# Performance work log

Hardware: AMD Instinct MI355X
Metric: run time of the kernel (lower is better)

## Reference

```python
import jax, jax.numpy as jnp
import numpy as np

N = 50000
E = 800000
F0, F1, F2 = 256, 128, 64
EPS = 1e-5


def setup_inputs() -> dict:
    key = jax.random.key(0)
    ks = jax.random.split(key, 20)
    x = jax.random.normal(ks[0], (N, F0), dtype=jnp.float32)
    src = jax.random.randint(ks[1], (E,), 0, N)
    dst = jax.random.randint(ks[2], (E,), 0, N)
    edge_index = jnp.stack([src, dst]).astype(jnp.int64)

    def lin(k, fi, fo):
        s = 1.0 / np.sqrt(fi)
        k1, k2 = jax.random.split(k)
        W = jax.random.uniform(k1, (fi, fo), minval=-s, maxval=s, dtype=jnp.float32)
        b = jax.random.uniform(k2, (fo,), minval=-s, maxval=s, dtype=jnp.float32)
        return W, b

    We1, be1 = lin(ks[3], F0, F1)
    We2, be2 = lin(ks[4], F1, F2)
    Wd1, bd1 = lin(ks[5], F2, F1)
    Wd2, bd2 = lin(ks[6], F1, F0)
    return {
        'x': x, 'edge_index': edge_index,
        'We1': We1, 'be1': be1, 'g1': jnp.ones((F1,)), 'bb1': jnp.zeros((F1,)),
        'We2': We2, 'be2': be2, 'g2': jnp.ones((F2,)), 'bb2': jnp.zeros((F2,)),
        'Wd1': Wd1, 'bd1': bd1, 'g3': jnp.ones((F1,)), 'bb3': jnp.zeros((F1,)),
        'Wd2': Wd2, 'bd2': bd2, 'g4': jnp.ones((F0,)), 'bb4': jnp.zeros((F0,)),
    }


def _gcn(x, W, b, src, dst, dinv_src_dst, dinv_self):
    # PyG GCNConv: linear first, then sym-normalized propagation with self-loops
    h = x @ W + b                               # [N, Fout]
    msg = h[src] * dinv_src_dst[:, None]        # [E, Fout]
    out = jax.ops.segment_sum(msg, dst, num_segments=N)
    return out + h * dinv_self[:, None]         # self-loop term


def _bn(x, g, b):
    # BatchNorm1d training-mode: biased batch stats over node dim
    m = jnp.mean(x, axis=0)
    v = jnp.mean(jnp.square(x - m), axis=0)
    return g * (x - m) * jax.lax.rsqrt(v + EPS) + b


def reference(x, edge_index, We1, be1, g1, bb1, We2, be2, g2, bb2,
              Wd1, bd1, g3, bb3, Wd2, bd2, g4, bb4):
    src, dst = edge_index[0], edge_index[1]
    deg = jnp.zeros((N,), x.dtype).at[dst].add(1.0) + 1.0  # in-degree + self-loop
    dinv = jax.lax.rsqrt(deg)
    dsd = dinv[src] * dinv[dst]
    dself = dinv * dinv

    relu = jax.nn.relu
    # Encoder block 0 (outer i==0): relu(GCN), relu(BN)
    h = relu(_gcn(x, We1, be1, src, dst, dsd, dself))
    h = relu(_bn(h, g1, bb1))
    enc1 = h
    # Encoder block 1 (outer i==1 == len(inner)-1): relu(GCN), BN (no relu)
    h = relu(_gcn(h, We2, be2, src, dst, dsd, dself))
    h = _bn(h, g2, bb2)
    enc2 = h
    # Decoder block 0: relu(GCN), relu(BN)
    h = relu(_gcn(h, Wd1, bd1, src, dst, dsd, dself))
    h = relu(_bn(h, g3, bb3))
    # Decoder block 1 (i==1): relu(GCN), BN (no relu)
    h = relu(_gcn(h, Wd2, bd2, src, dst, dsd, dself))
    h = _bn(h, g4, bb4)
    # AE returns (reconstruction, encoded_embeddings)
    return h, enc1, enc2
```

## Files before the change

kernel.cpp:

```cpp
#include <hip/hip_runtime.h>
#include <hip/hip_fp16.h>

#define N_NODES 50000
#define F0 256
#define F1 128
#define F2 64
#define BN_EPS 1e-5f

typedef float f32x4 __attribute__((ext_vector_type(4)));
typedef __bf16 bf16x8 __attribute__((ext_vector_type(8)));
typedef unsigned short ushort8v __attribute__((ext_vector_type(8)));

__device__ __forceinline__ float bflo(unsigned v) { return __uint_as_float(v << 16); }
__device__ __forceinline__ float bfhi(unsigned v) { return __uint_as_float(v & 0xFFFF0000u); }
__device__ __forceinline__ unsigned short f2bf(float f) {
  unsigned u = __float_as_uint(f);
  u += 0x7FFFu + ((u >> 16) & 1u);
  return (unsigned short)(u >> 16);
}
__device__ __forceinline__ void split2(float a, unsigned short& hi, unsigned short& lo) {
  hi = f2bf(a);
  float hf = __uint_as_float((unsigned)hi << 16);
  lo = f2bf(a - hf);
}
__device__ __forceinline__ int rdl(int v, int l) { return __builtin_amdgcn_readlane(v, l); }
__device__ __forceinline__ float h2f(unsigned short h) {
  __half hh = *reinterpret_cast<__half*>(&h);
  return __half2float(hh);
}
__device__ __forceinline__ unsigned short f2h(float f) {
  __half hh = __float2half(f);
  return *reinterpret_cast<unsigned short*>(&hh);
}

__global__ void count_dst(const int* __restrict__ dst, int* __restrict__ counts,
                          int* __restrict__ eslot, int E) {
  int e = blockIdx.x * blockDim.x + threadIdx.x;
  if (e < E) eslot[e] = atomicAdd(&counts[dst[e]], 1);
}

__global__ __launch_bounds__(256) void scan_blocks(const int* __restrict__ counts,
                                                   int* __restrict__ offs,
                                                   int* __restrict__ bsum,
                                                   float* __restrict__ dinv) {
  __shared__ int s_w[4];
  const int tid = threadIdx.x, lane = tid & 63, wid = tid >> 6;
  const int base = blockIdx.x * 1024 + tid * 4;
  int v0 = 0, v1 = 0, v2 = 0, v3 = 0;
  if (base + 3 < N_NODES) {
    int4 v = *(const int4*)(counts + base);
    v0 = v.x; v1 = v.y; v2 = v.z; v3 = v.w;
  } else if (base < N_NODES) {
    v0 = counts[base];
    if (base + 1 < N_NODES) v1 = counts[base + 1];
    if (base + 2 < N_NODES) v2 = counts[base + 2];
  }
  if (base < N_NODES) {
    dinv[base] = rsqrtf((float)v0 + 1.0f);
    if (base + 1 < N_NODES) dinv[base + 1] = rsqrtf((float)v1 + 1.0f);
    if (base + 2 < N_NODES) dinv[base + 2] = rsqrtf((float)v2 + 1.0f);
    if (base + 3 < N_NODES) dinv[base + 3] = rsqrtf((float)v3 + 1.0f);
  }
  int t = v0 + v1 + v2 + v3;
  int incl = t;
#pragma unroll
  for (int d = 1; d < 64; d <<= 1) {
    int x = __shfl_up(incl, d);
    if (lane >= d) incl += x;
  }
  if (lane == 63) s_w[wid] = incl;
  __syncthreads();
  int woff = 0;
#pragma unroll
  for (int j = 0; j < 4; j++)
    if (j < wid) woff += s_w[j];
  int p = woff + incl - t;
  if (base < N_NODES) offs[base] = p;
  p += v0;
  if (base + 1 < N_NODES) offs[base + 1] = p;
  p += v1;
  if (base + 2 < N_NODES) offs[base + 2] = p;
  p += v2;
  if (base + 3 < N_NODES) offs[base + 3] = p;
  if (tid == 255) bsum[blockIdx.x] = woff + incl;
}

__global__ void scan_tops(int* __restrict__ bsum, int* __restrict__ offs, int nblk) {
  int lane = threadIdx.x;
  int v = (lane < nblk) ? bsum[lane] : 0;
  int incl = v;
#pragma unroll
  for (int d = 1; d < 64; d <<= 1) {
    int x = __shfl_up(incl, d);
    if (lane >= d) incl += x;
  }
  if (lane < nblk) bsum[lane] = incl - v;
  if (lane == 63) offs[N_NODES] = incl;
}

__global__ __launch_bounds__(256) void scan_add(int* __restrict__ offs,
                                                const int* __restrict__ bsum) {
  const int add = bsum[blockIdx.x];
  const int base = blockIdx.x * 1024 + threadIdx.x * 4;
  if (base + 3 < N_NODES) {
    int4 v = *(const int4*)(offs + base);
    v.x += add; v.y += add; v.z += add; v.w += add;
    *(int4*)(offs + base) = v;
  } else if (base < N_NODES) {
    offs[base] += add;
    if (base + 1 < N_NODES) offs[base + 1] += add;
    if (base + 2 < N_NODES) offs[base + 2] += add;
  }
}

__global__ void fill_csr(const int* __restrict__ src, const int* __restrict__ dst,
                         const int* __restrict__ offs, const int* __restrict__ eslot,
                         const float* __restrict__ dinv,
                         unsigned* __restrict__ csrU, int E) {
  int e = blockIdx.x * blockDim.x + threadIdx.x;
  if (e < E) {
    int s = src[e], d = dst[e];
    int p = offs[d] + eslot[e];
    unsigned ent = (unsigned)s | ((unsigned)f2h(dinv[s]) << 16);
    __builtin_nontemporal_store(ent, &csrU[p]);
  }
}

__global__ void compute_rowsum(const int* __restrict__ offs,
                               const unsigned* __restrict__ csrU,
                               const float* __restrict__ dinv, float* __restrict__ rowsum) {
  int i = blockIdx.x * blockDim.x + threadIdx.x;
  if (i < N_NODES) {
    float di = dinv[i];
    float s = di;
    int e1 = offs[i + 1];
    for (int e = offs[i]; e < e1; e++) s += h2f((unsigned short)(csrU[e] >> 16));
    rowsum[i] = di * s;
  }
}

__device__ __forceinline__ void wt_one(const float* W, unsigned short* Wh, unsigned short* Wl,
                                       int K, int N, int idx) {
  int k = idx / N, n = idx - k * N;
  unsigned short h, l;
  split2(W[idx], h, l);
  Wh[(size_t)n * K + k] = h;
  Wl[(size_t)n * K + k] = l;
}

__global__ void convert_weights(const float* __restrict__ We1, const float* __restrict__ We2,
                                const float* __restrict__ Wd1, const float* __restrict__ Wd2,
                                unsigned short* W1h, unsigned short* W1l,
                                unsigned short* W2h, unsigned short* W2l,
                                unsigned short* W3h, unsigned short* W3l,
                                unsigned short* W4h, unsigned short* W4l) {
  int idx = blockIdx.x * blockDim.x + threadIdx.x;
  if (idx < 32768) {
    wt_one(We1, W1h, W1l, 256, 128, idx);
  } else if (idx < 40960) {
    wt_one(We2, W2h, W2l, 128, 64, idx - 32768);
  } else if (idx < 49152) {
    wt_one(Wd1, W3h, W3l, 64, 128, idx - 40960);
  } else if (idx < 81920) {
    wt_one(Wd2, W4h, W4l, 128, 256, idx - 49152);
  }
}

template <int BN, bool STATS, bool AF32>
__global__ __launch_bounds__(256) void mfma_gemm_split(
    const unsigned short* __restrict__ Ahi, const unsigned short* __restrict__ Alo,
    const float* __restrict__ Af,
    const unsigned short* __restrict__ Whi, const unsigned short* __restrict__ Wlo,
    const float* __restrict__ bias, const float* __restrict__ rowsum,
    unsigned short* __restrict__ Cb, float* __restrict__ Cf,
    float* __restrict__ spart, int M, int K, int N) {
  constexpr int BM = 128;
  constexpr int MT = (BN == 128) ? 4 : 2;
  constexpr int NT = 4;
  __shared__ __align__(16) unsigned short AsH[4][BM][8];
  __shared__ __align__(16) unsigned short AsL[4][BM][8];
  __shared__ __align__(16) unsigned short BsH[4][BN][8];
  __shared__ __align__(16) unsigned short BsL[4][BN][8];
  __shared__ float sls[BN], slq[BN];
  const int tid = threadIdx.x;
  const int lane = tid & 63, wid = tid >> 6;
  const int quad = lane >> 4, ln = lane & 15;
  const int m0 = blockIdx.x * BM;
  const int n0 = blockIdx.y * BN;
  const int wm = (BN == 128) ? (wid & 1) * 64 : wid * 32;
  const int wn = (BN == 128) ? (wid >> 1) * 64 : 0;
  f32x4 acc[MT][NT] = {};
  if (STATS && tid < BN) {
    sls[tid] = 0.f;
    slq[tid] = 0.f;
  }

  const int arow = tid >> 2, aseg = tid & 3;
  for (int k0 = 0; k0 < K; k0 += 32) {
#pragma unroll
    for (int i = 0; i < 2; i++) {
      int row = arow + i * 64;
      int gm = m0 + row;
      if (AF32) {
        float4 u0 = make_float4(0.f, 0.f, 0.f, 0.f), u1 = u0;
        if (gm < M) {
          u0 = *(const float4*)(Af + (size_t)gm * K + k0 + aseg * 8);
          u1 = *(const float4*)(Af + (size_t)gm * K + k0 + aseg * 8 + 4);
        }
        ushort4 h0, l0, h1, l1;
        split2(u0.x, h0.x, l0.x); split2(u0.y, h0.y, l0.y);
        split2(u0.z, h0.z, l0.z); split2(u0.w, h0.w, l0.w);
        split2(u1.x, h1.x, l1.x); split2(u1.y, h1.y, l1.y);
        split2(u1.z, h1.z, l1.z); split2(u1.w, h1.w, l1.w);
        *(ushort4*)(&AsH[aseg][row][0]) = h0;
        *(ushort4*)(&AsH[aseg][row][4]) = h1;
        *(ushort4*)(&AsL[aseg][row][0]) = l0;
        *(ushort4*)(&AsL[aseg][row][4]) = l1;
      } else {
        ushort8v vh = {0, 0, 0, 0, 0, 0, 0, 0};
        ushort8v vl = {0, 0, 0, 0, 0, 0, 0, 0};
        if (gm < M) {
          vh = *(const ushort8v*)(Ahi + (size_t)gm * K + k0 + aseg * 8);
          vl = *(const ushort8v*)(Alo + (size_t)gm * K + k0 + aseg * 8);
        }
        *(ushort8v*)(&AsH[aseg][row][0]) = vh;
        *(ushort8v*)(&AsL[aseg][row][0]) = vl;
      }
    }
#pragma unroll
    for (int i = 0; i < BN / 64; i++) {
      int n = arow + i * 64;
      *(ushort8v*)(&BsH[aseg][n][0]) =
          *(const ushort8v*)(Whi + (size_t)(n0 + n) * K + k0 + aseg * 8);
      *(ushort8v*)(&BsL[aseg][n][0]) =
          *(const ushort8v*)(Wlo + (size_t)(n0 + n) * K + k0 + aseg * 8);
    }
    __syncthreads();
    bf16x8 ah[MT], al[MT], bh[NT], bl[NT];
#pragma unroll
    for (int mt = 0; mt < MT; mt++) {
      ah[mt] = *(const bf16x8*)(&AsH[quad][wm + mt * 16 + ln][0]);
      al[mt] = *(const bf16x8*)(&AsL[quad][wm + mt * 16 + ln][0]);
    }
#pragma unroll
    for (int nt = 0; nt < NT; nt++) {
      bh[nt] = *(const bf16x8*)(&BsH[quad][wn + nt * 16 + ln][0]);
      bl[nt] = *(const bf16x8*)(&BsL[quad][wn + nt * 16 + ln][0]);
    }
#pragma unroll
    for (int mt = 0; mt < MT; mt++)
#pragma unroll
      for (int nt = 0; nt < NT; nt++) {
        acc[mt][nt] = __builtin_amdgcn_mfma_f32_16x16x32_bf16(ah[mt], bl[nt], acc[mt][nt], 0, 0, 0);
        acc[mt][nt] = __builtin_amdgcn_mfma_f32_16x16x32_bf16(al[mt], bh[nt], acc[mt][nt], 0, 0, 0);
        acc[mt][nt] = __builtin_amdgcn_mfma_f32_16x16x32_bf16(ah[mt], bh[nt], acc[mt][nt], 0, 0, 0);
      }
    __syncthreads();
  }

  if (!STATS) {
#pragma unroll
    for (int nt = 0; nt < NT; nt++) {
      int gn = n0 + wn + nt * 16 + ln;
      float bv = bias[gn];
#pragma unroll
      for (int mt = 0; mt < MT; mt++) {
#pragma unroll
        for (int r = 0; r < 4; r++) {
          int gm = m0 + wm + mt * 16 + quad * 4 + r;
          if (gm < M) Cb[(size_t)gm * N + gn] = f2bf(acc[mt][nt][r] + bv);
        }
      }
    }
  } else {
    float rs[MT][4];
#pragma unroll
    for (int mt = 0; mt < MT; mt++)
#pragma unroll
      for (int r = 0; r < 4; r++) {
        int gm = m0 + wm + mt * 16 + quad * 4 + r;
        rs[mt][r] = (gm < M) ? rowsum[gm] : 0.f;
      }
#pragma unroll
    for (int nt = 0; nt < NT; nt++) {
      int gn = n0 + wn + nt * 16 + ln;
      float bv = bias[gn];
      float ls = 0.f, lq = 0.f;
#pragma unroll
      for (int mt = 0; mt < MT; mt++) {
#pragma unroll
        for (int r = 0; r < 4; r++) {
          int gm = m0 + wm + mt * 16 + quad * 4 + r;
          if (gm < M) {
            float v = fmaxf(fmaf(bv, rs[mt][r], acc[mt][nt][r]), 0.f);
            Cf[(size_t)gm * N + gn] = v;
            ls += v;
            lq = fmaf(v, v, lq);
          }
        }
      }
      ls += __shfl_xor(ls, 16); ls += __shfl_xor(ls, 32);
      lq += __shfl_xor(lq, 16); lq += __shfl_xor(lq, 32);
      if (quad == 0) {
        atomicAdd(&sls[wn + nt * 16 + ln], ls);
        atomicAdd(&slq[wn + nt * 16 + ln], lq);
      }
    }
    __syncthreads();
    if (tid < BN) {
      size_t base = (size_t)blockIdx.x * (2 * N);
      spart[base + n0 + tid] = sls[tid];
      spart[base + N + n0 + tid] = slq[tid];
    }
  }
}

__global__ __launch_bounds__(256) void reduce_stats(const float* __restrict__ spart,
                                                    float* __restrict__ stat, int nbx, int N) {
  const int c = blockIdx.x;
  const int t = threadIdx.x;
  const int N2 = 2 * N;
  float ls = 0.f, lq = 0.f;
  for (int b = t; b < nbx; b += 256) {
    ls += spart[(size_t)b * N2 + c];
    lq += spart[(size_t)b * N2 + N + c];
  }
#pragma unroll
  for (int d = 1; d < 64; d <<= 1) {
    ls += __shfl_xor(ls, d);
    lq += __shfl_xor(lq, d);
  }
  __shared__ float rl[4], rq[4];
  if ((t & 63) == 0) {
    rl[t >> 6] = ls;
    rq[t >> 6] = lq;
  }
  __syncthreads();
  if (t == 0) {
    stat[c] = rl[0] + rl[1] + rl[2] + rl[3];
    stat[256 + c] = rq[0] + rq[1] + rq[2] + rq[3];
  }
}

template <bool RELU_STATS, bool OUT_SPLIT>
__global__ __launch_bounds__(256) void agg128_rl(
    const unsigned short* __restrict__ hb, const int* __restrict__ offs,
    const unsigned* __restrict__ csrU, const float* __restrict__ dinv,
    float* __restrict__ outf, unsigned short* __restrict__ outhi,
    unsigned short* __restrict__ outlo, float* __restrict__ stat) {
  const int tid = threadIdx.x;
  const int lane = tid & 63;
  const int widx = tid >> 6;
  const int nwaves = gridDim.x * 4;
  float ls0 = 0.f, ls1 = 0.f, lq0 = 0.f, lq1 = 0.f;

  for (int node = blockIdx.x * 4 + widx; node < N_NODES; node += nwaves) {
    const int e0 = __builtin_amdgcn_readfirstlane(offs[node]);
    const int e1 = __builtin_amdgcn_readfirstlane(offs[node + 1]);
    float a0 = 0.f, a1 = 0.f;
    for (int e = e0; e < e1; e += 64) {
      const int cnt = min(64, e1 - e);
      unsigned ent = 0;
      if (lane < cnt) ent = csrU[e + lane];
      const int nb = (cnt + 7) & ~7;
      for (int j = 0; j < nb; j += 8) {
#pragma unroll
        for (int u = 0; u < 8; u++) {
          unsigned ce = (unsigned)rdl((int)ent, j + u);
          int s = (int)(ce & 0xFFFFu);
          float w = h2f((unsigned short)(ce >> 16));
          unsigned v = *(const unsigned*)(hb + (size_t)s * 128 + lane * 2);
          a0 = fmaf(bflo(v), w, a0);
          a1 = fmaf(bfhi(v), w, a1);
        }
      }
    }
    float di = dinv[node];
    unsigned vs = *(const unsigned*)(hb + (size_t)node * 128 + lane * 2);
    a0 = fmaf(bflo(vs), di, a0) * di;
    a1 = fmaf(bfhi(vs), di, a1) * di;
    if (RELU_STATS) {
      a0 = fmaxf(a0, 0.f);
      a1 = fmaxf(a1, 0.f);
      ls0 += a0; ls1 += a1;
      lq0 = fmaf(a0, a0, lq0);
      lq1 = fmaf(a1, a1, lq1);
    }
    if (OUT_SPLIT) {
      unsigned short h0, l0, h1, l1;
      split2(a0, h0, l0);
      split2(a1, h1, l1);
      *(unsigned*)(outhi + (size_t)node * 128 + lane * 2) = (unsigned)h0 | ((unsigned)h1 << 16);
      *(unsigned*)(outlo + (size_t)node * 128 + lane * 2) = (unsigned)l0 | ((unsigned)l1 << 16);
    } else {
      *(float2*)(outf + (size_t)node * 128 + lane * 2) = make_float2(a0, a1);
    }
  }

  if (RELU_STATS) {
    __shared__ float red[4][128];
    red[widx][lane * 2 + 0] = ls0;
    red[widx][lane * 2 + 1] = ls1;
    __syncthreads();
    if (tid < 128) {
      atomicAdd(&stat[tid], red[0][tid] + red[1][tid] + red[2][tid] + red[3][tid]);
    }
    __syncthreads();
    red[widx][lane * 2 + 0] = lq0;
    red[widx][lane * 2 + 1] = lq1;
    __syncthreads();
    if (tid < 128) {
      atomicAdd(&stat[256 + tid], red[0][tid] + red[1][tid] + red[2][tid] + red[3][tid]);
    }
  }
}

template <bool RELU_STATS, bool OUT_SPLIT>
__global__ __launch_bounds__(256) void agg64_rl(
    const unsigned short* __restrict__ hb, const int* __restrict__ offs,
    const unsigned* __restrict__ csrU, const float* __restrict__ dinv,
    float* __restrict__ outf, unsigned short* __restrict__ outhi,
    unsigned short* __restrict__ outlo, float* __restrict__ stat) {
  const int tid = threadIdx.x;
  const int lane = tid & 63;
  const int widx = tid >> 6;
  const int half = lane >> 5;
  const int hl = lane & 31;
  const int nwaves = gridDim.x * 4;
  float ls0 = 0.f, ls1 = 0.f, lq0 = 0.f, lq1 = 0.f;

  for (int node = blockIdx.x * 4 + widx; node < N_NODES; node += nwaves) {
    const int e0 = __builtin_amdgcn_readfirstlane(offs[node]);
    const int e1 = __builtin_amdgcn_readfirstlane(offs[node + 1]);
    float a0 = 0.f, a1 = 0.f;
    for (int e = e0; e < e1; e += 64) {
      const int cnt = min(64, e1 - e);
      unsigned ent = 0;
      if (lane < cnt) ent = csrU[e + lane];
      const int nb = (cnt + 15) & ~15;
      for (int j = 0; j < nb; j += 16) {
#pragma unroll
        for (int u = 0; u < 8; u++) {
          unsigned ca = (unsigned)rdl((int)ent, j + 2 * u);
          unsigned cb = (unsigned)rdl((int)ent, j + 2 * u + 1);
          unsigned ce = half ? cb : ca;
          int s = (int)(ce & 0xFFFFu);
          float w = h2f((unsigned short)(ce >> 16));
          unsigned v = *(const unsigned*)(hb + (size_t)s * 64 + hl * 2);
          a0 = fmaf(bflo(v), w, a0);
          a1 = fmaf(bfhi(v), w, a1);
        }
      }
    }
    a0 += __shfl_xor(a0, 32);
    a1 += __shfl_xor(a1, 32);
    float di = dinv[node];
    unsigned vs = *(const unsigned*)(hb + (size_t)node * 64 + hl * 2);
    a0 = fmaf(bflo(vs), di, a0) * di;
    a1 = fmaf(bfhi(vs), di, a1) * di;
    if (RELU_STATS) {
      a0 = fmaxf(a0, 0.f);
      a1 = fmaxf(a1, 0.f);
      if (half == 0) {
        ls0 += a0; ls1 += a1;
        lq0 = fmaf(a0, a0, lq0);
        lq1 = fmaf(a1, a1, lq1);
      }
    }
    if (half == 0) {
      if (OUT_SPLIT) {
        unsigned short h0, l0, h1, l1;
        split2(a0, h0, l0);
        split2(a1, h1, l1);
        *(unsigned*)(outhi + (size_t)node * 64 + hl * 2) = (unsigned)h0 | ((unsigned)h1 << 16);
        *(unsigned*)(outlo + (size_t)node * 64 + hl * 2) = (unsigned)l0 | ((unsigned)l1 << 16);
      } else {
        *(float2*)(outf + (size_t)node * 64 + hl * 2) = make_float2(a0, a1);
      }
    }
  }

  if (RELU_STATS) {
    __shared__ float red[4][64];
    if (half == 0) {
      red[widx][hl * 2 + 0] = ls0;
      red[widx][hl * 2 + 1] = ls1;
    }
    __syncthreads();
    if (tid < 64) {
      atomicAdd(&stat[tid], red[0][tid] + red[1][tid] + red[2][tid] + red[3][tid]);
    }
    __syncthreads();
    if (half == 0) {
      red[widx][hl * 2 + 0] = lq0;
      red[widx][hl * 2 + 1] = lq1;
    }
    __syncthreads();
    if (tid < 64) {
      atomicAdd(&stat[256 + tid], red[0][tid] + red[1][tid] + red[2][tid] + red[3][tid]);
    }
  }
}

template <int F, bool RELU, bool WF32, bool WB16, bool WSPLIT>
__global__ __launch_bounds__(256) void bn_apply_f(const float* __restrict__ a,
                                                  const float* __restrict__ stat,
                                                  const float* __restrict__ g,
                                                  const float* __restrict__ bb,
                                                  float* __restrict__ outf,
                                                  unsigned short* __restrict__ outb,
                                                  unsigned short* __restrict__ outhi,
                                                  unsigned short* __restrict__ outlo) {
  __shared__ float s_scale[F], s_shift[F];
  const int tid = threadIdx.x;
  if (tid < F) {
    const float invN = 1.0f / (float)N_NODES;
    float mean = stat[tid] * invN;
    float var = fmaxf(stat[256 + tid] * invN - mean * mean, 0.f);
    float inv = rsqrtf(var + BN_EPS);
    float sc = g[tid] * inv;
    s_scale[tid] = sc;
    s_shift[tid] = bb[tid] - mean * sc;
  }
  __syncthreads();
  constexpr int C4 = F / 4;
  const int total = N_NODES * C4;
  for (int idx = blockIdx.x * blockDim.x + tid; idx < total; idx += gridDim.x * blockDim.x) {
    int c4 = idx % C4;
    float4 v = ((const float4*)a)[idx];
    float4 s = *(float4*)&s_scale[c4 * 4];
    float4 sh = *(float4*)&s_shift[c4 * 4];
    float4 o;
    o.x = fmaf(v.x, s.x, sh.x);
    o.y = fmaf(v.y, s.y, sh.y);
    o.z = fmaf(v.z, s.z, sh.z);
    o.w = fmaf(v.w, s.w, sh.w);
    if (RELU) {
      o.x = fmaxf(o.x, 0.f);
      o.y = fmaxf(o.y, 0.f);
      o.z = fmaxf(o.z, 0.f);
      o.w = fmaxf(o.w, 0.f);
    }
    if (WF32) ((float4*)outf)[idx] = o;
    if (WB16) {
      ushort4 b;
      b.x = f2bf(o.x); b.y = f2bf(o.y); b.z = f2bf(o.z); b.w = f2bf(o.w);
      ((ushort4*)outb)[idx] = b;
    }
    if (WSPLIT) {
      ushort4 h, l;
      split2(o.x, h.x, l.x);
      split2(o.y, h.y, l.y);
      split2(o.z, h.z, l.z);
      split2(o.w, h.w, l.w);
      ((ushort4*)outhi)[idx] = h;
      ((ushort4*)outlo)[idx] = l;
    }
  }
}

extern "C" void kernel_launch(void* const* d_in, const int* in_sizes, int n_in,
                              void* d_out, int out_size, void* d_ws, size_t ws_size,
                              hipStream_t stream) {
  const float* x = (const float*)d_in[0];
  const int* ei = (const int*)d_in[1];
  const int E = in_sizes[1] / 2;
  const int* src = ei;
  const int* dst = ei + E;
  const float* We1 = (const float*)d_in[2];  const float* be1 = (const float*)d_in[3];
  const float* g1  = (const float*)d_in[4];  const float* bb1 = (const float*)d_in[5];
  const float* We2 = (const float*)d_in[6];  const float* be2 = (const float*)d_in[7];
  const float* g2  = (const float*)d_in[8];  const float* bb2 = (const float*)d_in[9];
  const float* Wd1 = (const float*)d_in[10]; const float* bd1 = (const float*)d_in[11];
  const float* g3  = (const float*)d_in[12]; const float* bb3 = (const float*)d_in[13];
  const float* Wd2 = (const float*)d_in[14]; const float* bd2 = (const float*)d_in[15];
  const float* g4  = (const float*)d_in[16]; const float* bb4 = (const float*)d_in[17];

  float* out = (float*)d_out;
  char* ws = (char*)d_ws;
  unsigned short* A0b  = (unsigned short*)(ws + 0);
  unsigned short* A1b  = (unsigned short*)(ws + 12800000);
  unsigned short* C2b  = (unsigned short*)(ws + 32000000);
  unsigned short* G3hi = (unsigned short*)(ws + 0);
  unsigned short* G3lo = (unsigned short*)(ws + 6400000);
  unsigned short* D3b  = (unsigned short*)(ws + 12800000);
  unsigned short* G4hi = (unsigned short*)(ws + 0);
  unsigned short* G4lo = (unsigned short*)(ws + 25600000);
  unsigned short* Wb   = (unsigned short*)(ws + 48000000);
  unsigned short* W1h = Wb;            unsigned short* W1l = W1h + 32768;
  unsigned short* W2h = W1l + 32768;   unsigned short* W2l = W2h + 8192;
  unsigned short* W3h = W2l + 8192;    unsigned short* W3l = W3h + 8192;
  unsigned short* W4h = W3l + 8192;    unsigned short* W4l = W4h + 32768;
  float* B0f  = (float*)(ws + 51200000);
  int*   eslot  = (int*)(ws + 51200000);
  unsigned* csrU = (unsigned*)(ws + 102400000);
  float* spart  = (float*)(ws + 105600000);
  float* stat4  = (float*)(ws + 108800000);
  int*   bsum   = (int*)(ws + 108808192);
  int*   counts = (int*)(ws + 108810000);
  int*   offs   = (int*)(ws + 109210000);
  float* dinv   = (float*)(ws + 109410064);
  if (ws_size < 109604160) return;
  float* rowsum = (float*)counts;

  float* enc1 = out + (size_t)N_NODES * F0;
  float* enc2 = enc1 + (size_t)N_NODES * F1;

  const int EB = (E + 255) / 256;
  const int AGG_GRID = 2048;
  const int MB = (N_NODES + 127) / 128;
  const int SCAN_B = (N_NODES + 1023) / 1024;

  convert_weights<<<320, 256, 0, stream>>>(We1, We2, Wd1, Wd2, W1h, W1l, W2h, W2l,
                                           W3h, W3l, W4h, W4l);
  hipMemsetAsync(counts, 0, N_NODES * sizeof(int), stream);
  hipMemsetAsync(stat4, 0, 4 * 512 * sizeof(float), stream);
  count_dst<<<EB, 256, 0, stream>>>(dst, counts, eslot, E);
  scan_blocks<<<SCAN_B, 256, 0, stream>>>(counts, offs, bsum, dinv);
  scan_tops<<<1, 64, 0, stream>>>(bsum, offs, SCAN_B);
  scan_add<<<SCAN_B, 256, 0, stream>>>(offs, bsum);
  fill_csr<<<EB, 256, 0, stream>>>(src, dst, offs, eslot, dinv, csrU, E);
  compute_rowsum<<<(N_NODES + 255) / 256, 256, 0, stream>>>(offs, csrU, dinv, rowsum);

  mfma_gemm_split<128, false, true><<<dim3(MB, 1), 256, 0, stream>>>(
      nullptr, nullptr, x, W1h, W1l, be1, nullptr, A0b, nullptr, nullptr, N_NODES, F0, F1);
  agg128_rl<true, false><<<AGG_GRID, 256, 0, stream>>>(
      A0b, offs, csrU, dinv, B0f, nullptr, nullptr, stat4);
  bn_apply_f<F1, true, true, false, false><<<2048, 256, 0, stream>>>(
      B0f, stat4, g1, bb1, enc1, nullptr, nullptr, nullptr);

  mfma_gemm_split<64, false, true><<<dim3(MB, 1), 256, 0, stream>>>(
      nullptr, nullptr, enc1, W2h, W2l, be2, nullptr, A1b, nullptr, nullptr, N_NODES, F1, F2);
  agg64_rl<true, false><<<AGG_GRID, 256, 0, stream>>>(
      A1b, offs, csrU, dinv, B0f, nullptr, nullptr, stat4 + 512);
  bn_apply_f<F2, false, true, true, false><<<2048, 256, 0, stream>>>(
      B0f, stat4 + 512, g2, bb2, enc2, C2b, nullptr, nullptr);

  agg64_rl<false, true><<<AGG_GRID, 256, 0, stream>>>(
      C2b, offs, csrU, dinv, nullptr, G3hi, G3lo, nullptr);
  mfma_gemm_split<128, true, false><<<dim3(MB, 1), 256, 0, stream>>>(
      G3hi, G3lo, nullptr, W3h, W3l, bd1, rowsum, nullptr, B0f, spart, N_NODES, F2, F1);
  reduce_stats<<<F1, 256, 0, stream>>>(spart, stat4 + 1024, MB, F1);
  bn_apply_f<F1, true, false, true, false><<<2048, 256, 0, stream>>>(
      B0f, stat4 + 1024, g3, bb3, nullptr, D3b, nullptr, nullptr);

  agg128_rl<false, true><<<AGG_GRID, 256, 0, stream>>>(
      D3b, offs, csrU, dinv, nullptr, G4hi, G4lo, nullptr);
  mfma_gemm_split<128, true, false><<<dim3(MB, 2), 256, 0, stream>>>(
      G4hi, G4lo, nullptr, W4h, W4l, bd2, rowsum, nullptr, B0f, spart, N_NODES, F1, F0);
  reduce_stats<<<F0, 256, 0, stream>>>(spart, stat4 + 1536, MB, F0);
  bn_apply_f<F0, false, true, false, false><<<2048, 256, 0, stream>>>(
      B0f, stat4 + 1536, g4, bb4, out, nullptr, nullptr, nullptr);
}
```

Baseline: 566.1 us.

## Fuse CSR fill, rowsum and BN1 apply into adjacent GEMM/aggregation kernels

The CSR fill now runs in extra blocks appended to the first GEMM launch, and the rowsum computation runs in extra blocks appended to the first 128-wide aggregation. The first BatchNorm+ReLU is applied while the second GEMM loads its input, which also writes enc1, so the separate bn_apply pass is removed. This cuts three launches and one full read/write pass over the 128-wide activation. The cost is extra per-element work in the GEMM load path and heterogeneous blocks sharing a grid.

```diff
diff --git a/kernel.cpp b/kernel.cpp
--- a/kernel.cpp
+++ b/kernel.cpp
@@ -113,32 +113,6 @@
   }
 }
 
-__global__ void fill_csr(const int* __restrict__ src, const int* __restrict__ dst,
-                         const int* __restrict__ offs, const int* __restrict__ eslot,
-                         const float* __restrict__ dinv,
-                         unsigned* __restrict__ csrU, int E) {
-  int e = blockIdx.x * blockDim.x + threadIdx.x;
-  if (e < E) {
-    int s = src[e], d = dst[e];
-    int p = offs[d] + eslot[e];
-    unsigned ent = (unsigned)s | ((unsigned)f2h(dinv[s]) << 16);
-    __builtin_nontemporal_store(ent, &csrU[p]);
-  }
-}
-
-__global__ void compute_rowsum(const int* __restrict__ offs,
-                               const unsigned* __restrict__ csrU,
-                               const float* __restrict__ dinv, float* __restrict__ rowsum) {
-  int i = blockIdx.x * blockDim.x + threadIdx.x;
-  if (i < N_NODES) {
-    float di = dinv[i];
-    float s = di;
-    int e1 = offs[i + 1];
-    for (int e = offs[i]; e < e1; e++) s += h2f((unsigned short)(csrU[e] >> 16));
-    rowsum[i] = di * s;
-  }
-}
-
 __device__ __forceinline__ void wt_one(const float* W, unsigned short* Wh, unsigned short* Wl,
                                        int K, int N, int idx) {
   int k = idx / N, n = idx - k * N;
@@ -166,23 +140,40 @@
   }
 }
 
-template <int BN, bool STATS, bool AF32>
+template <int BN, bool STATS, bool AF32, bool BNIN, bool FILL>
 __global__ __launch_bounds__(256) void mfma_gemm_split(
     const unsigned short* __restrict__ Ahi, const unsigned short* __restrict__ Alo,
     const float* __restrict__ Af,
     const unsigned short* __restrict__ Whi, const unsigned short* __restrict__ Wlo,
     const float* __restrict__ bias, const float* __restrict__ rowsum,
     unsigned short* __restrict__ Cb, float* __restrict__ Cf,
-    float* __restrict__ spart, int M, int K, int N) {
+    float* __restrict__ spart, int M, int K, int N,
+    const float* __restrict__ bnstat, const float* __restrict__ bng,
+    const float* __restrict__ bnb, float* __restrict__ Aout,
+    const int* __restrict__ fsrc, const int* __restrict__ fdst,
+    const int* __restrict__ foffs, const int* __restrict__ feslot,
+    const float* __restrict__ fdinv, unsigned* __restrict__ fcsr, int fE, int gemmBX) {
   constexpr int BM = 128;
   constexpr int MT = (BN == 128) ? 4 : 2;
   constexpr int NT = 4;
+  const int tid = threadIdx.x;
+  if (FILL && (int)blockIdx.x >= gemmBX) {
+    int idx = ((int)blockIdx.x - gemmBX) * 256 + tid;
+    int stride = ((int)gridDim.x - gemmBX) * 256;
+    for (int e = idx; e < fE; e += stride) {
+      int s = fsrc[e], d = fdst[e];
+      int p = foffs[d] + feslot[e];
+      unsigned ent = (unsigned)s | ((unsigned)f2h(fdinv[s]) << 16);
+      __builtin_nontemporal_store(ent, &fcsr[p]);
+    }
+    return;
+  }
   __shared__ __align__(16) unsigned short AsH[4][BM][8];
   __shared__ __align__(16) unsigned short AsL[4][BM][8];
   __shared__ __align__(16) unsigned short BsH[4][BN][8];
   __shared__ __align__(16) unsigned short BsL[4][BN][8];
-  __shared__ float sls[BN], slq[BN];
-  const int tid = threadIdx.x;
+  __shared__ float sls[STATS ? BN : 1], slq[STATS ? BN : 1];
+  __shared__ float s_bsc[BNIN ? 256 : 1], s_bsh[BNIN ? 256 : 1];
   const int lane = tid & 63, wid = tid >> 6;
   const int quad = lane >> 4, ln = lane & 15;
   const int m0 = blockIdx.x * BM;
@@ -194,6 +185,18 @@
     sls[tid] = 0.f;
     slq[tid] = 0.f;
   }
+  if (BNIN) {
+    if (tid < K) {
+      const float invN = 1.0f / (float)N_NODES;
+      float mean = bnstat[tid] * invN;
+      float var = fmaxf(bnstat[256 + tid] * invN - mean * mean, 0.f);
+      float inv = rsqrtf(var + BN_EPS);
+      float sc = bng[tid] * inv;
+      s_bsc[tid] = sc;
+      s_bsh[tid] = bnb[tid] - mean * sc;
+    }
+    __syncthreads();
+  }
 
   const int arow = tid >> 2, aseg = tid & 3;
   for (int k0 = 0; k0 < K; k0 += 32) {
@@ -206,6 +209,19 @@
         if (gm < M) {
           u0 = *(const float4*)(Af + (size_t)gm * K + k0 + aseg * 8);
           u1 = *(const float4*)(Af + (size_t)gm * K + k0 + aseg * 8 + 4);
+          if (BNIN) {
+            int c = k0 + aseg * 8;
+            u0.x = fmaxf(fmaf(u0.x, s_bsc[c + 0], s_bsh[c + 0]), 0.f);
+            u0.y = fmaxf(fmaf(u0.y, s_bsc[c + 1], s_bsh[c + 1]), 0.f);
+            u0.z = fmaxf(fmaf(u0.z, s_bsc[c + 2], s_bsh[c + 2]), 0.f);
+            u0.w = fmaxf(fmaf(u0.w, s_bsc[c + 3], s_bsh[c + 3]), 0.f);
+            u1.x = fmaxf(fmaf(u1.x, s_bsc[c + 4], s_bsh[c + 4]), 0.f);
+            u1.y = fmaxf(fmaf(u1.y, s_bsc[c + 5], s_bsh[c + 5]), 0.f);
+            u1.z = fmaxf(fmaf(u1.z, s_bsc[c + 6], s_bsh[c + 6]), 0.f);
+            u1.w = fmaxf(fmaf(u1.w, s_bsc[c + 7], s_bsh[c + 7]), 0.f);
+            *(float4*)(Aout + (size_t)gm * K + c) = u0;
+            *(float4*)(Aout + (size_t)gm * K + c + 4) = u1;
+          }
         }
         ushort4 h0, l0, h1, l1;
         split2(u0.x, h0.x, l0.x); split2(u0.y, h0.y, l0.y);
@@ -342,16 +358,29 @@
   }
 }
 
-template <bool RELU_STATS, bool OUT_SPLIT>
+template <bool RELU_STATS, bool OUT_SPLIT, bool ROWSUM>
 __global__ __launch_bounds__(256) void agg128_rl(
     const unsigned short* __restrict__ hb, const int* __restrict__ offs,
     const unsigned* __restrict__ csrU, const float* __restrict__ dinv,
     float* __restrict__ outf, unsigned short* __restrict__ outhi,
-    unsigned short* __restrict__ outlo, float* __restrict__ stat) {
+    unsigned short* __restrict__ outlo, float* __restrict__ stat,
+    float* __restrict__ rowsum_out, int aggBX) {
   const int tid = threadIdx.x;
+  if (ROWSUM && (int)blockIdx.x >= aggBX) {
+    int i = ((int)blockIdx.x - aggBX) * 256 + tid;
+    int stride = ((int)gridDim.x - aggBX) * 256;
+    for (; i < N_NODES; i += stride) {
+      float di = dinv[i];
+      float s = di;
+      int e1 = offs[i + 1];
+      for (int e = offs[i]; e < e1; e++) s += h2f((unsigned short)(csrU[e] >> 16));
+      rowsum_out[i] = di * s;
+    }
+    return;
+  }
   const int lane = tid & 63;
   const int widx = tid >> 6;
-  const int nwaves = gridDim.x * 4;
+  const int nwaves = aggBX * 4;
   float ls0 = 0.f, ls1 = 0.f, lq0 = 0.f, lq1 = 0.f;
 
   for (int node = blockIdx.x * 4 + widx; node < N_NODES; node += nwaves) {
@@ -610,6 +639,8 @@
   const int AGG_GRID = 2048;
   const int MB = (N_NODES + 127) / 128;
   const int SCAN_B = (N_NODES + 1023) / 1024;
+  const int FB = 512;
+  const int RB = 196;
 
   convert_weights<<<320, 256, 0, stream>>>(We1, We2, Wd1, Wd2, W1h, W1l, W2h, W2l,
                                            W3h, W3l, W4h, W4l);
@@ -619,18 +650,18 @@
   scan_blocks<<<SCAN_B, 256, 0, stream>>>(counts, offs, bsum, dinv);
   scan_tops<<<1, 64, 0, stream>>>(bsum, offs, SCAN_B);
   scan_add<<<SCAN_B, 256, 0, stream>>>(offs, bsum);
-  fill_csr<<<EB, 256, 0, stream>>>(src, dst, offs, eslot, dinv, csrU, E);
-  compute_rowsum<<<(N_NODES + 255) / 256, 256, 0, stream>>>(offs, csrU, dinv, rowsum);
-
-  mfma_gemm_split<128, false, true><<<dim3(MB, 1), 256, 0, stream>>>(
-      nullptr, nullptr, x, W1h, W1l, be1, nullptr, A0b, nullptr, nullptr, N_NODES, F0, F1);
-  agg128_rl<true, false><<<AGG_GRID, 256, 0, stream>>>(
-      A0b, offs, csrU, dinv, B0f, nullptr, nullptr, stat4);
-  bn_apply_f<F1, true, true, false, false><<<2048, 256, 0, stream>>>(
-      B0f, stat4, g1, bb1, enc1, nullptr, nullptr, nullptr);
-
-  mfma_gemm_split<64, false, true><<<dim3(MB, 1), 256, 0, stream>>>(
-      nullptr, nullptr, enc1, W2h, W2l, be2, nullptr, A1b, nullptr, nullptr, N_NODES, F1, F2);
+
+  mfma_gemm_split<128, false, true, false, true><<<dim3(MB + FB, 1), 256, 0, stream>>>(
+      nullptr, nullptr, x, W1h, W1l, be1, nullptr, A0b, nullptr, nullptr, N_NODES, F0, F1,
+      nullptr, nullptr, nullptr, nullptr,
+      src, dst, offs, eslot, dinv, csrU, E, MB);
+  agg128_rl<true, false, true><<<AGG_GRID + RB, 256, 0, stream>>>(
+      A0b, offs, csrU, dinv, B0f, nullptr, nullptr, stat4, rowsum, AGG_GRID);
+
+  mfma_gemm_split<64, false, true, true, false><<<dim3(MB, 1), 256, 0, stream>>>(
+      nullptr, nullptr, B0f, W2h, W2l, be2, nullptr, A1b, nullptr, nullptr, N_NODES, F1, F2,
+      stat4, g1, bb1, enc1,
+      nullptr, nullptr, nullptr, nullptr, nullptr, nullptr, 0, 0);
   agg64_rl<true, false><<<AGG_GRID, 256, 0, stream>>>(
       A1b, offs, csrU, dinv, B0f, nullptr, nullptr, stat4 + 512);
   bn_apply_f<F2, false, true, true, false><<<2048, 256, 0, stream>>>(
@@ -638,16 +669,20 @@
 
   agg64_rl<false, true><<<AGG_GRID, 256, 0, stream>>>(
       C2b, offs, csrU, dinv, nullptr, G3hi, G3lo, nullptr);
-  mfma_gemm_split<128, true, false><<<dim3(MB, 1), 256, 0, stream>>>(
-      G3hi, G3lo, nullptr, W3h, W3l, bd1, rowsum, nullptr, B0f, spart, N_NODES, F2, F1);
+  mfma_gemm_split<128, true, false, false, false><<<dim3(MB, 1), 256, 0, stream>>>(
+      G3hi, G3lo, nullptr, W3h, W3l, bd1, rowsum, nullptr, B0f, spart, N_NODES, F2, F1,
+      nullptr, nullptr, nullptr, nullptr,
+      nullptr, nullptr, nullptr, nullptr, nullptr, nullptr, 0, 0);
   reduce_stats<<<F1, 256, 0, stream>>>(spart, stat4 + 1024, MB, F1);
   bn_apply_f<F1, true, false, true, false><<<2048, 256, 0, stream>>>(
       B0f, stat4 + 1024, g3, bb3, nullptr, D3b, nullptr, nullptr);
 
-  agg128_rl<false, true><<<AGG_GRID, 256, 0, stream>>>(
-      D3b, offs, csrU, dinv, nullptr, G4hi, G4lo, nullptr);
-  mfma_gemm_split<128, true, false><<<dim3(MB, 2), 256, 0, stream>>>(
-      G4hi, G4lo, nullptr, W4h, W4l, bd2, rowsum, nullptr, B0f, spart, N_NODES, F1, F0);
+  agg128_rl<false, true, false><<<AGG_GRID, 256, 0, stream>>>(
+      D3b, offs, csrU, dinv, nullptr, G4hi, G4lo, nullptr, nullptr, AGG_GRID);
+  mfma_gemm_split<128, true, false, false, false><<<dim3(MB, 2), 256, 0, stream>>>(
+      G4hi, G4lo, nullptr, W4h, W4l, bd2, rowsum, nullptr, B0f, spart, N_NODES, F1, F0,
+      nullptr, nullptr, nullptr, nullptr,
+      nullptr, nullptr, nullptr, nullptr, nullptr, nullptr, 0, 0);
   reduce_stats<<<F0, 256, 0, stream>>>(spart, stat4 + 1536, MB, F0);
   bn_apply_f<F0, false, true, false, false><<<2048, 256, 0, stream>>>(
       B0f, stat4 + 1536, g4, bb4, out, nullptr, nullptr, nullptr);
```

Measured after the change: 545.4 us. 3.6% less time.
